# Kernel optimization log

Hardware: AMD Instinct MI355X
Metric: run time of the kernel (lower is better)

## Reference

```python
import jax, jax.numpy as jnp
import numpy as np
import math

B, N, F_IN, F_OUT = 16, 2048, 256, 64


def setup_inputs() -> dict:
    key = jax.random.key(0)
    k1, k2, k3, k4 = jax.random.split(key, 4)
    x = jax.random.normal(k1, (B, N, F_IN), dtype=jnp.float32)
    adj = jax.random.randint(k2, (B, N, N), 0, 2, dtype=jnp.int32)
    stdv = 1.0 / math.sqrt(F_OUT)
    weight = jax.random.uniform(k3, (F_IN, F_OUT), dtype=jnp.float32, minval=-stdv, maxval=stdv)
    # weight2 stdv = 1/sqrt(1) = 1.0
    weight2 = jax.random.uniform(k4, (2 * F_OUT, 1), dtype=jnp.float32, minval=-1.0, maxval=1.0)
    return {"x": x, "adj": adj, "weight": weight, "weight2": weight2}


def reference(x, adj, weight, weight2):
    # h[b,n,o] = (x @ weight)  -- shared linear projection
    h = jnp.einsum("bni,io->bno", x, weight)
    Fo = weight.shape[1]
    # Split additive-attention vector: e_ij = relu(h_i . a_src + h_j . a_dst)
    # Mathematically identical to cat([h_i, h_j]) @ weight2 of the original.
    a_src = weight2[:Fo, 0]
    a_dst = weight2[Fo:, 0]
    s_src = jnp.einsum("bno,o->bn", h, a_src)  # [B, N]
    s_dst = jnp.einsum("bno,o->bn", h, a_dst)  # [B, N]
    e = jax.nn.relu(s_src[:, :, None] + s_dst[:, None, :])  # [B, N, N]
    NEG = jnp.float32(-9e15)
    scores = jnp.where(adj > 0, e, NEG)
    attention = jax.nn.softmax(scores, axis=2)  # softmax over neighbors j
    # dropout = 0.0 / eval mode -> identity
    out = jnp.einsum("bij,bjo->bio", attention, h)  # [B, N, F_OUT]
    return out
```

## Files before the change

kernel.cpp:

```cpp
#include <hip/hip_runtime.h>
#include <hip/hip_bf16.h>

#define BB 16
#define NN 2048
#define FIN 256
#define FO 64

typedef __bf16 bf16x8 __attribute__((ext_vector_type(8)));
typedef float  f32x4  __attribute__((ext_vector_type(4)));
typedef int    i32x4  __attribute__((ext_vector_type(4)));
typedef unsigned int uint;

__global__ __launch_bounds__(256) void k1_gemm(
    const float* __restrict__ x, const float* __restrict__ weight,
    const float* __restrict__ w2,
    __bf16* __restrict__ hT, float* __restrict__ s_src, float* __restrict__ s_dst) {
    __shared__ __bf16 WtL[FO * 264];
    __shared__ float vsL[FIN], vdL[FIN];
    int t = threadIdx.x;
    {
        const float4* wr = (const float4*)(weight + t * FO);
        float a = 0.f, d = 0.f;
#pragma unroll
        for (int c = 0; c < 16; ++c) {
            float4 v = wr[c];
            int o = c * 4;
            WtL[(o + 0) * 264 + t] = (__bf16)v.x;
            WtL[(o + 1) * 264 + t] = (__bf16)v.y;
            WtL[(o + 2) * 264 + t] = (__bf16)v.z;
            WtL[(o + 3) * 264 + t] = (__bf16)v.w;
            a += v.x * w2[o] + v.y * w2[o + 1] + v.z * w2[o + 2] + v.w * w2[o + 3];
            d += v.x * w2[FO + o] + v.y * w2[FO + o + 1] +
                 v.z * w2[FO + o + 2] + v.w * w2[FO + o + 3];
        }
        vsL[t] = a;
        vdL[t] = d;
    }
    __syncthreads();

    int lane = threadIdx.x & 63, w = threadIdx.x >> 6;
    int quad = lane >> 4, m = lane & 15;
    int Rbase = blockIdx.x * 64 + w * 16;
    int R = Rbase + m;
    const float* xr = x + (long)R * FIN;

    f32x4 acc[4] = {};
    float ps = 0.f, pd = 0.f;

#pragma unroll
    for (int k0 = 0; k0 < FIN; k0 += 32) {
        int kb = k0 + quad * 8;
        float4 x0 = *(const float4*)(xr + kb);
        float4 x1 = *(const float4*)(xr + kb + 4);
        float4 u0 = *(const float4*)(vsL + kb);
        float4 u1 = *(const float4*)(vsL + kb + 4);
        float4 t0 = *(const float4*)(vdL + kb);
        float4 t1 = *(const float4*)(vdL + kb + 4);
        ps += x0.x * u0.x + x0.y * u0.y + x0.z * u0.z + x0.w * u0.w +
              x1.x * u1.x + x1.y * u1.y + x1.z * u1.z + x1.w * u1.w;
        pd += x0.x * t0.x + x0.y * t0.y + x0.z * t0.z + x0.w * t0.w +
              x1.x * t1.x + x1.y * t1.y + x1.z * t1.z + x1.w * t1.w;
        bf16x8 bf = {(__bf16)x0.x, (__bf16)x0.y, (__bf16)x0.z, (__bf16)x0.w,
                     (__bf16)x1.x, (__bf16)x1.y, (__bf16)x1.z, (__bf16)x1.w};
#pragma unroll
        for (int ot = 0; ot < 4; ++ot) {
            bf16x8 af = *(const bf16x8*)(WtL + (ot * 16 + m) * 264 + kb);
            acc[ot] = __builtin_amdgcn_mfma_f32_16x16x32_bf16(af, bf, acc[ot], 0, 0, 0);
        }
    }
    ps += __shfl_xor(ps, 16);
    ps += __shfl_xor(ps, 32);
    pd += __shfl_xor(pd, 16);
    pd += __shfl_xor(pd, 32);
    if (quad == 0) {
        s_src[R] = ps;
        s_dst[R] = pd;
    }
    int b = R >> 11;
    int nb = Rbase & (NN - 1);
#pragma unroll
    for (int ot = 0; ot < 4; ++ot) {
#pragma unroll
        for (int r = 0; r < 4; ++r) {
            int o = ot * 16 + quad * 4 + r;
            hT[((long)b * FO + o) * NN + nb + m] = (__bf16)acc[ot][r];
        }
    }
}

__global__ __launch_bounds__(256, 2) void k2_attn(
    const int* __restrict__ adj, const float* __restrict__ s_src,
    const float* __restrict__ s_dst, const __bf16* __restrict__ hT,
    float* __restrict__ out) {
    __shared__ float EL[NN];
    int b = blockIdx.x >> 5;
    int i0 = (blockIdx.x & 31) << 6;
    int lane = threadIdx.x & 63, w = threadIdx.x >> 6;
    int quad = lane >> 4, m = lane & 15;
    int rowbase = i0 + w * 16;
    int row = rowbase + m;

    const float* sd = s_dst + b * NN;
    float mx = -3.0e38f;
    for (int j = lane; j < NN; j += 64) mx = fmaxf(mx, sd[j]);
#pragma unroll
    for (int off = 32; off >= 1; off >>= 1) mx = fmaxf(mx, __shfl_xor(mx, off));
    for (int t = lane; t < NN; t += 64) EL[t] = __expf(sd[t] - mx);

    float ssr = s_src[b * NN + row];
    float T = ssr + mx;
    float M = fmaxf(T, 0.f);
    float K = __expf(fminf(T, 0.f));
    float cM = __expf(-M);

    const int* adjrow = adj + ((long)(b * NN + row)) * NN;
    const __bf16* hTb = hT + (long)b * FO * NN;
    int q8 = quad * 8;

    f32x4 acc[4] = {};
    f32x4 accL = {};
    const bf16x8 ones = {(__bf16)1.f, (__bf16)1.f, (__bf16)1.f, (__bf16)1.f,
                         (__bf16)1.f, (__bf16)1.f, (__bf16)1.f, (__bf16)1.f};
    uint bw[16];

#pragma unroll
    for (int g = 0; g < 4; ++g) {
#pragma unroll
        for (int ii = 0; ii < 4; ++ii) {
            int i = g * 4 + ii;
            uint bwv = 0;
#pragma unroll
            for (int j = 0; j < 4; ++j) {
                int ks = i * 4 + j;
                const i32x4* ap = (const i32x4*)(adjrow + ks * 32 + q8);
                i32x4 a0 = __builtin_nontemporal_load(ap);
                i32x4 a1 = __builtin_nontemporal_load(ap + 1);
                uint by = (uint)(a0.x > 0) | ((uint)(a0.y > 0) << 1) |
                          ((uint)(a0.z > 0) << 2) | ((uint)(a0.w > 0) << 3) |
                          ((uint)(a1.x > 0) << 4) | ((uint)(a1.y > 0) << 5) |
                          ((uint)(a1.z > 0) << 6) | ((uint)(a1.w > 0) << 7);
                bwv |= by << (8 * j);
            }
            bw[i] = bwv;
        }
#pragma unroll
        for (int u = 0; u < 16; ++u) {
            int ks = g * 16 + u;
            uint mb = (bw[g * 4 + (u >> 2)] >> ((u & 3) * 8)) & 0xffu;
            const float* ep = EL + ks * 32 + q8;
            float4 e0 = *(const float4*)ep;
            float4 e1 = *(const float4*)(ep + 4);
            float p0 = (mb & 1u)   ? fmaxf(K * e0.x, cM) : 0.f;
            float p1 = (mb & 2u)   ? fmaxf(K * e0.y, cM) : 0.f;
            float p2 = (mb & 4u)   ? fmaxf(K * e0.z, cM) : 0.f;
            float p3 = (mb & 8u)   ? fmaxf(K * e0.w, cM) : 0.f;
            float p4 = (mb & 16u)  ? fmaxf(K * e1.x, cM) : 0.f;
            float p5 = (mb & 32u)  ? fmaxf(K * e1.y, cM) : 0.f;
            float p6 = (mb & 64u)  ? fmaxf(K * e1.z, cM) : 0.f;
            float p7 = (mb & 128u) ? fmaxf(K * e1.w, cM) : 0.f;
            bf16x8 af = {(__bf16)p0, (__bf16)p1, (__bf16)p2, (__bf16)p3,
                         (__bf16)p4, (__bf16)p5, (__bf16)p6, (__bf16)p7};
            accL = __builtin_amdgcn_mfma_f32_16x16x32_bf16(af, ones, accL, 0, 0, 0);
            const __bf16* hb = hTb + ks * 32 + q8;
#pragma unroll
            for (int ot = 0; ot < 4; ++ot) {
                bf16x8 bf = *(const bf16x8*)(hb + (ot * 16 + m) * NN);
                acc[ot] = __builtin_amdgcn_mfma_f32_16x16x32_bf16(af, bf, acc[ot], 0, 0, 0);
            }
        }
    }

    float* outp = out + ((long)b * NN + rowbase) * FO;
#pragma unroll
    for (int r = 0; r < 4; ++r) {
        int orow = quad * 4 + r;
        float inv = 1.0f / accL[r];
#pragma unroll
        for (int ot = 0; ot < 4; ++ot) {
            outp[(long)orow * FO + ot * 16 + m] = acc[ot][r] * inv;
        }
    }
}

extern "C" void kernel_launch(void* const* d_in, const int* in_sizes, int n_in,
                              void* d_out, int out_size, void* d_ws, size_t ws_size,
                              hipStream_t stream) {
    const float* x      = (const float*)d_in[0];
    const int*   adj    = (const int*)d_in[1];
    const float* weight = (const float*)d_in[2];
    const float* w2     = (const float*)d_in[3];
    float* out = (float*)d_out;

    char* ws = (char*)d_ws;
    __bf16* hT   = (__bf16*)ws;
    float* s_src = (float*)(ws + 4194304);
    float* s_dst = (float*)(ws + 4194304 + 131072);

    k1_gemm<<<512, 256, 0, stream>>>(x, weight, w2, hT, s_src, s_dst);
    k2_attn<<<512, 256, 0, stream>>>(adj, s_src, s_dst, hT, out);
}
```

Baseline: 437.6 us.

## Pre-pack adjacency into a bitmask in a separate streaming pass

Adds extra blocks to the first kernel that read the int32 adjacency with wide, fully parallel streaming loads and pack each group of 8 entries into one byte of a bitmask in workspace. The attention kernel then reads compact 16-byte mask chunks per row instead of loading and comparing int32 adjacency inline, which should lighten its memory pressure at its limited occupancy. It also simplifies the per-element softmax numerator to max(e, exp(-T)), a per-row rescale that cancels in normalization. The cost is an extra 8 MB mask write and read, a much larger grid, and a possibly larger intermediate magnitude when T is very negative.

```diff
diff --git a/kernel.cpp b/kernel.cpp
--- a/kernel.cpp
+++ b/kernel.cpp
@@ -11,10 +11,23 @@
 typedef int    i32x4  __attribute__((ext_vector_type(4)));
 typedef unsigned int uint;
 
-__global__ __launch_bounds__(256) void k1_gemm(
+__global__ __launch_bounds__(256) void k_pre(
     const float* __restrict__ x, const float* __restrict__ weight,
-    const float* __restrict__ w2,
-    __bf16* __restrict__ hT, float* __restrict__ s_src, float* __restrict__ s_dst) {
+    const float* __restrict__ w2, const int* __restrict__ adj,
+    __bf16* __restrict__ hT, float* __restrict__ s_src, float* __restrict__ s_dst,
+    unsigned char* __restrict__ mask) {
+    if (blockIdx.x >= 512) {
+        size_t t = (size_t)(blockIdx.x - 512) * 256 + threadIdx.x;
+        const i32x4* ap = (const i32x4*)(adj + t * 8);
+        i32x4 a0 = __builtin_nontemporal_load(ap);
+        i32x4 a1 = __builtin_nontemporal_load(ap + 1);
+        unsigned bb = (unsigned)(a0.x > 0) | ((unsigned)(a0.y > 0) << 1) |
+                      ((unsigned)(a0.z > 0) << 2) | ((unsigned)(a0.w > 0) << 3) |
+                      ((unsigned)(a1.x > 0) << 4) | ((unsigned)(a1.y > 0) << 5) |
+                      ((unsigned)(a1.z > 0) << 6) | ((unsigned)(a1.w > 0) << 7);
+        mask[t] = (unsigned char)bb;
+        return;
+    }
     __shared__ __bf16 WtL[FO * 264];
     __shared__ float vsL[FIN], vdL[FIN];
     int t = threadIdx.x;
@@ -89,7 +102,7 @@
 }
 
 __global__ __launch_bounds__(256, 2) void k2_attn(
-    const int* __restrict__ adj, const float* __restrict__ s_src,
+    const unsigned char* __restrict__ mask, const float* __restrict__ s_src,
     const float* __restrict__ s_dst, const __bf16* __restrict__ hT,
     float* __restrict__ out) {
     __shared__ float EL[NN];
@@ -107,13 +120,10 @@
     for (int off = 32; off >= 1; off >>= 1) mx = fmaxf(mx, __shfl_xor(mx, off));
     for (int t = lane; t < NN; t += 64) EL[t] = __expf(sd[t] - mx);
 
-    float ssr = s_src[b * NN + row];
-    float T = ssr + mx;
-    float M = fmaxf(T, 0.f);
-    float K = __expf(fminf(T, 0.f));
-    float cM = __expf(-M);
+    float T = s_src[b * NN + row] + mx;
+    float cK = __expf(-T);
 
-    const int* adjrow = adj + ((long)(b * NN + row)) * NN;
+    const uint4* mrow = (const uint4*)(mask + ((size_t)(b * NN + row)) * 256);
     const __bf16* hTb = hT + (long)b * FO * NN;
     int q8 = quad * 8;
 
@@ -121,43 +131,30 @@
     f32x4 accL = {};
     const bf16x8 ones = {(__bf16)1.f, (__bf16)1.f, (__bf16)1.f, (__bf16)1.f,
                          (__bf16)1.f, (__bf16)1.f, (__bf16)1.f, (__bf16)1.f};
-    uint bw[16];
 
 #pragma unroll
     for (int g = 0; g < 4; ++g) {
-#pragma unroll
-        for (int ii = 0; ii < 4; ++ii) {
-            int i = g * 4 + ii;
-            uint bwv = 0;
-#pragma unroll
-            for (int j = 0; j < 4; ++j) {
-                int ks = i * 4 + j;
-                const i32x4* ap = (const i32x4*)(adjrow + ks * 32 + q8);
-                i32x4 a0 = __builtin_nontemporal_load(ap);
-                i32x4 a1 = __builtin_nontemporal_load(ap + 1);
-                uint by = (uint)(a0.x > 0) | ((uint)(a0.y > 0) << 1) |
-                          ((uint)(a0.z > 0) << 2) | ((uint)(a0.w > 0) << 3) |
-                          ((uint)(a1.x > 0) << 4) | ((uint)(a1.y > 0) << 5) |
-                          ((uint)(a1.z > 0) << 6) | ((uint)(a1.w > 0) << 7);
-                bwv |= by << (8 * j);
-            }
-            bw[i] = bwv;
-        }
+        uint4 mv0 = mrow[g * 4 + 0];
+        uint4 mv1 = mrow[g * 4 + 1];
+        uint4 mv2 = mrow[g * 4 + 2];
+        uint4 mv3 = mrow[g * 4 + 3];
+        uint mg[16] = {mv0.x, mv0.y, mv0.z, mv0.w, mv1.x, mv1.y, mv1.z, mv1.w,
+                       mv2.x, mv2.y, mv2.z, mv2.w, mv3.x, mv3.y, mv3.z, mv3.w};
 #pragma unroll
         for (int u = 0; u < 16; ++u) {
             int ks = g * 16 + u;
-            uint mb = (bw[g * 4 + (u >> 2)] >> ((u & 3) * 8)) & 0xffu;
+            uint mb = (mg[u] >> (q8)) & 0xffu;
             const float* ep = EL + ks * 32 + q8;
             float4 e0 = *(const float4*)ep;
             float4 e1 = *(const float4*)(ep + 4);
-            float p0 = (mb & 1u)   ? fmaxf(K * e0.x, cM) : 0.f;
-            float p1 = (mb & 2u)   ? fmaxf(K * e0.y, cM) : 0.f;
-            float p2 = (mb & 4u)   ? fmaxf(K * e0.z, cM) : 0.f;
-            float p3 = (mb & 8u)   ? fmaxf(K * e0.w, cM) : 0.f;
-            float p4 = (mb & 16u)  ? fmaxf(K * e1.x, cM) : 0.f;
-            float p5 = (mb & 32u)  ? fmaxf(K * e1.y, cM) : 0.f;
-            float p6 = (mb & 64u)  ? fmaxf(K * e1.z, cM) : 0.f;
-            float p7 = (mb & 128u) ? fmaxf(K * e1.w, cM) : 0.f;
+            float p0 = (mb & 1u)   ? fmaxf(e0.x, cK) : 0.f;
+            float p1 = (mb & 2u)   ? fmaxf(e0.y, cK) : 0.f;
+            float p2 = (mb & 4u)   ? fmaxf(e0.z, cK) : 0.f;
+            float p3 = (mb & 8u)   ? fmaxf(e0.w, cK) : 0.f;
+            float p4 = (mb & 16u)  ? fmaxf(e1.x, cK) : 0.f;
+            float p5 = (mb & 32u)  ? fmaxf(e1.y, cK) : 0.f;
+            float p6 = (mb & 64u)  ? fmaxf(e1.z, cK) : 0.f;
+            float p7 = (mb & 128u) ? fmaxf(e1.w, cK) : 0.f;
             bf16x8 af = {(__bf16)p0, (__bf16)p1, (__bf16)p2, (__bf16)p3,
                          (__bf16)p4, (__bf16)p5, (__bf16)p6, (__bf16)p7};
             accL = __builtin_amdgcn_mfma_f32_16x16x32_bf16(af, ones, accL, 0, 0, 0);
@@ -195,7 +192,8 @@
     __bf16* hT   = (__bf16*)ws;
     float* s_src = (float*)(ws + 4194304);
     float* s_dst = (float*)(ws + 4194304 + 131072);
+    unsigned char* mask = (unsigned char*)(ws + 4194304 + 262144);
 
-    k1_gemm<<<512, 256, 0, stream>>>(x, weight, w2, hT, s_src, s_dst);
-    k2_attn<<<512, 256, 0, stream>>>(adj, s_src, s_dst, hT, out);
+    k_pre<<<33280, 256, 0, stream>>>(x, weight, w2, adj, hT, s_src, s_dst, mask);
+    k2_attn<<<512, 256, 0, stream>>>(mask, s_src, s_dst, hT, out);
 }
```

New measurement: 449.4 us. 1.03x slower.
